# Kernel tuning notes

Measured on AMD Instinct MI355X. Metric: run time of the kernel, lower is better.

## Reference

```python
import jax, jax.numpy as jnp
import numpy as np

B, C, H, W = 8, 128, 64, 64
NWIN, HEADS, QKDIM, KVPW, TOPK = 8, 8, 128, 4, 16
SCALE = QKDIM ** -0.5

def _ln(x, g, b, eps):
    mu = x.mean(-1, keepdims=True)
    var = ((x - mu) ** 2).mean(-1, keepdims=True)
    return (x - mu) * jax.lax.rsqrt(var + eps) * g + b

def _conv(x, w, b, pad, groups=1):
    y = jax.lax.conv_general_dilated(x, w, (1, 1), [(pad, pad), (pad, pad)],
        dimension_numbers=('NCHW', 'OIHW', 'NCHW'), feature_group_count=groups)
    return y + b[None, :, None, None]

def setup_inputs():
    key = jax.random.key(0)
    ks = jax.random.split(key, 8)
    s = 0.05
    return {
        't1': jax.random.normal(ks[0], (B, C, H, W), jnp.float32),
        't2': jax.random.normal(ks[1], (B, C, H, W), jnp.float32),
        'pos_w': jax.random.normal(ks[2], (C, 1, 3, 3), jnp.float32) * s,
        'pos_b': jnp.zeros((C,), jnp.float32),
        'cat_w': jax.random.normal(ks[3], (C, 2 * C, 3, 3), jnp.float32) * s,
        'cat_b': jnp.zeros((C,), jnp.float32),
        'ln_cat_g': jnp.ones((C,), jnp.float32),
        'ln_cat_b': jnp.zeros((C,), jnp.float32),
        'ln1_g': jnp.ones((C,), jnp.float32),
        'ln1_b': jnp.zeros((C,), jnp.float32),
        'qkv_w': jax.random.normal(ks[4], (2 * QKDIM + C, C), jnp.float32) * s,
        'qkv_b': jnp.zeros((2 * QKDIM + C,), jnp.float32),
        'lepe_w': jax.random.normal(ks[5], (C, 1, 5, 5), jnp.float32) * s,
        'lepe_b': jnp.zeros((C,), jnp.float32),
        'wo_w': jax.random.normal(ks[6], (C, C), jnp.float32) * s,
        'wo_b': jnp.zeros((C,), jnp.float32),
    }

def _bra_cross(q_in, kv_in, qkv_w, qkv_b, lepe_w, lepe_b, wo_w, wo_b):
    # Bi-level routing cross attention: queries from q_in, keys/values from kv_in (NHWC).
    p = NWIN; wh, ww = H // p, W // p; p2 = p * p
    q = (q_in @ qkv_w.T + qkv_b)[..., :QKDIM]          # (B,H,W,QKDIM)
    kv = (kv_in @ qkv_w.T + qkv_b)[..., QKDIM:]        # (B,H,W,QKDIM+C)

    def win(x):
        c = x.shape[-1]
        return x.reshape(B, p, wh, p, ww, c).transpose(0, 1, 3, 2, 4, 5).reshape(B, p2, wh, ww, c)

    qw, kvw = win(q), win(kv)
    q_pix = qw.reshape(B, p2, wh * ww, QKDIM)
    # adaptive avg-pool each window's kv to KVPW x KVPW ('ada_avgpool')
    f = wh // KVPW
    kv_pix = kvw.reshape(B, p2, KVPW, f, KVPW, f, QKDIM + C).mean(axis=(3, 5))
    kv_pix = kv_pix.reshape(B, p2, KVPW * KVPW, QKDIM + C)
    q_win = qw.mean(axis=(2, 3))                        # (B,p2,QKDIM)
    k_win = kvw[..., :QKDIM].mean(axis=(2, 3))
    # LePE: depthwise 5x5 conv on full-resolution v
    v_full = kv[..., QKDIM:].transpose(0, 3, 1, 2)
    lepe = _conv(v_full, lepe_w, lepe_b, 2, groups=C).transpose(0, 2, 3, 1)
    # region-level routing (detached: diff_routing=False)
    logits = jnp.einsum('bpc,bqc->bpq',
                        jax.lax.stop_gradient(q_win) * SCALE,
                        jax.lax.stop_gradient(k_win))
    _, r_idx = jax.lax.top_k(logits, TOPK)              # (B,p2,TOPK)
    # gather kv of routed regions: (B,p2,TOPK,KVPW^2,QKDIM+C)
    kv_sel = jax.vmap(lambda kvp, idx: kvp[idx])(kv_pix, r_idx)
    k_sel = kv_sel[..., :QKDIM].reshape(B, p2, TOPK * KVPW * KVPW, HEADS, QKDIM // HEADS)
    v_sel = kv_sel[..., QKDIM:].reshape(B, p2, TOPK * KVPW * KVPW, HEADS, C // HEADS)
    q_h = q_pix.reshape(B, p2, wh * ww, HEADS, QKDIM // HEADS)
    attn = jnp.einsum('bpqmc,bpkmc->bpmqk', q_h * SCALE, k_sel)
    attn = jax.nn.softmax(attn, axis=-1)
    out = jnp.einsum('bpmqk,bpkmc->bpqmc', attn, v_sel).reshape(B, p2, wh, ww, C)
    out = out.reshape(B, p, p, wh, ww, C).transpose(0, 1, 3, 2, 4, 5).reshape(B, H, W, C)
    out = out + lepe
    return out @ wo_w.T + wo_b

def reference(t1, t2, pos_w, pos_b, cat_w, cat_b, ln_cat_g, ln_cat_b,
              ln1_g, ln1_b, qkv_w, qkv_b, lepe_w, lepe_b, wo_w, wo_b):
    # Block.forward: depthwise conv positional embedding
    t1 = t1 + _conv(t1, pos_w, pos_b, 1, groups=C)
    t2 = t2 + _conv(t2, pos_w, pos_b, 1, groups=C)
    t1n = t1.transpose(0, 2, 3, 1)
    t2n = t2.transpose(0, 2, 3, 1)
    # RGBConcatConv: cat on channel-last, 3x3 conv, relu(LayerNorm)
    xc = jnp.concatenate([t1n, t2n], axis=3).transpose(0, 3, 1, 2)
    xc = _conv(xc, cat_w, cat_b, 1).transpose(0, 2, 3, 1)
    x = jax.nn.relu(_ln(xc, ln_cat_g, ln_cat_b, 1e-5))
    attn = _bra_cross(_ln(t1n, ln1_g, ln1_b, 1e-6), _ln(t2n, ln1_g, ln1_b, 1e-6),
                      qkv_w, qkv_b, lepe_w, lepe_b, wo_w, wo_b)
    x = x + attn
    return x.transpose(0, 3, 1, 2)
```

## Files before the change

### kernel.cpp

```cpp
#include <hip/hip_runtime.h>
#include <math.h>

typedef unsigned short ushort_t;
typedef __attribute__((ext_vector_type(4))) float f32x4;
typedef __attribute__((ext_vector_type(16))) float f32x16;
typedef __attribute__((ext_vector_type(8))) short bf16x8;

constexpr int B = 8, C = 128, H = 64, W = 64;
constexpr int HEADS = 8, TOPK = 16;
constexpr int P2 = 64;
constexpr float SCALE = 0.0883883476483184405f;

constexpr size_t NPIX    = (size_t)B * H * W;
constexpr size_t OFF_T1C = 0;
constexpr size_t OFF_T2C = OFF_T1C + NPIX * 128;
constexpr size_t OFF_X   = OFF_T2C + NPIX * 128;
constexpr size_t OFF_QB  = OFF_X   + NPIX * 128;
constexpr size_t OFF_KV  = OFF_QB  + NPIX * 64;
constexpr size_t OFF_KVP = OFF_KV  + NPIX * 256;
constexpr size_t OFF_RW1 = OFF_KVP + 524288;
constexpr size_t OFF_RW2 = OFF_RW1 + 524288;
constexpr size_t OFF_KVPT= OFF_KVP + (size_t)B * P2 * 16 * 256;
constexpr size_t OFF_QW  = OFF_KVPT+ (size_t)B * P2 * 128 * 16 / 2;
constexpr size_t OFF_KW  = OFF_QW  + (size_t)B * P2 * 128;
constexpr size_t OFF_RIDX= OFF_KW  + (size_t)B * P2 * 128;
constexpr size_t OFF_WCB = OFF_RIDX+ (size_t)B * P2 * TOPK;
constexpr size_t OFF_QKVB= OFF_WCB + (size_t)9 * 256 * 128;
constexpr size_t OFF_WOB = OFF_QKVB+ (size_t)384 * 128 / 2;
constexpr size_t OFF_T1B = OFF_WOB + 8192;
constexpr size_t OFF_T2B = OFF_T1B + NPIX * 64;

__device__ inline ushort_t f2bf(float f) {
    unsigned u = __float_as_uint(f);
    unsigned r = u + 0x7FFFu + ((u >> 16) & 1u);
    return (ushort_t)(r >> 16);
}
__device__ inline float bf2f(ushort_t u) {
    return __uint_as_float((unsigned)u << 16);
}

__global__ __launch_bounds__(256) void prep_pos_k(
        const float* __restrict__ t1, const float* __restrict__ t2,
        const float* __restrict__ pos_w, const float* __restrict__ pos_b,
        const float* __restrict__ qkv_w, const float* __restrict__ wo_w,
        const float* __restrict__ cat_w,
        ushort_t* __restrict__ qkvB, ushort_t* __restrict__ woB,
        ushort_t* __restrict__ wcat2,
        float* __restrict__ out1, float* __restrict__ out2,
        ushort_t* __restrict__ ob1, ushort_t* __restrict__ ob2) {
    __shared__ float tile[4][32][33];
    int bid = blockIdx.x;
    int t = threadIdx.x;
    if (bid < 1152) {
        int idx = bid * 256 + t;
        if (idx < 384 * 128) qkvB[idx] = f2bf(qkv_w[idx]);
        if (idx < 128 * 128) woB[idx]  = f2bf(wo_w[idx]);
        if (idx < 36 * 8 * 128 * 8) {
            int i  = idx & 7;
            int n  = (idx >> 3) & 127;
            int r  = idx >> 10;
            int lg = r & 3;
            int kk = (r >> 2) & 1;
            int sdd = r >> 3;
            int dd = sdd % 9, q = sdd / 9;
            int ci = q * 64 + kk * 32 + lg * 8 + i;
            wcat2[idx] = f2bf(cat_w[((size_t)n * 256 + ci) * 9 + dd]);
        }
        return;
    }
    int pb = bid - 1152;
    int xb = pb & 1, cg = (pb >> 1) & 3, z = pb >> 3;
    int which = z >> 7, rem = z & 127;
    int b = rem >> 4, y0 = (rem & 15) * 4;
    const float* in = which ? t2 : t1;
    float* outNHWC = which ? out2 : out1;
    ushort_t* outB = which ? ob2 : ob1;
    int c0 = cg * 32, x0 = xb * 32;
    int tx = t & 31, tg = t >> 5;
    int x = x0 + tx;
    for (int i = 0; i < 4; i++) {
        int cl = tg * 4 + i, c = c0 + cl;
        const float* base = in + (size_t)(b * C + c) * H * W;
        float wv[9];
#pragma unroll
        for (int j = 0; j < 9; j++) wv[j] = pos_w[c * 9 + j];
        float rows[6][3];
#pragma unroll
        for (int yy = 0; yy < 6; yy++) {
            int gy = y0 - 1 + yy;
            bool yok = (gy >= 0 && gy < H);
#pragma unroll
            for (int dx = 0; dx < 3; dx++) {
                int gx = x + dx - 1;
                rows[yy][dx] = (yok && gx >= 0 && gx < W) ? base[gy * W + gx] : 0.f;
            }
        }
        float bb = pos_b[c];
#pragma unroll
        for (int k = 0; k < 4; k++) {
            float acc = rows[k + 1][1] + bb;
#pragma unroll
            for (int dy = 0; dy < 3; dy++)
#pragma unroll
                for (int dx = 0; dx < 3; dx++)
                    acc += rows[k + dy][dx] * wv[dy * 3 + dx];
            tile[k][cl][tx] = acc;
        }
    }
    __syncthreads();
    for (int k = 0; k < 4; k++)
        for (int i = 0; i < 4; i++) {
            int xl = tg * 4 + i;
            float val = tile[k][tx][xl];
            size_t idx = ((size_t)(b * H + y0 + k) * W + x0 + xl) * 128 + c0 + tx;
            outNHWC[idx] = val;
            outB[idx] = f2bf(val);
        }
}

__global__ __launch_bounds__(512) void cat_ln_k(
        const ushort_t* __restrict__ t1b, const ushort_t* __restrict__ t2b,
        const ushort_t* __restrict__ wcat2,
        const float* __restrict__ cat_b,
        const float* __restrict__ gcat, const float* __restrict__ bcat,
        ushort_t* __restrict__ xbuf,
        const float* __restrict__ t1c, const float* __restrict__ t2c,
        const float* __restrict__ g1, const float* __restrict__ b1,
        const ushort_t* __restrict__ qkvB, const float* __restrict__ qkv_b,
        ushort_t* __restrict__ outQ, ushort_t* __restrict__ outKV,
        float* __restrict__ rw1, float* __restrict__ rw2) {
    __shared__ __align__(16) unsigned char smem[64 * 272 * 2];
    int bid = blockIdx.x;
    int t = threadIdx.x;
    int lane = t & 63, wv = t >> 6;
    int l15 = lane & 15, lg = lane >> 4;

    if (bid < 512) {
        unsigned char* ash = smem;
        int which = bid >> 8;
        int blk = bid & 255;
        const float* in = which ? t2c : t1c;
        float* rw = which ? rw2 : rw1;
        size_t p0 = (size_t)blk * 128;
        int bb_ = blk >> 5, y0 = (blk & 31) * 2;
        {
            int row = t >> 2, sub = t & 3;
            const float* src = in + (p0 + row) * 128 + sub * 32;
            float4 v[8];
            float s = 0.f;
#pragma unroll
            for (int j = 0; j < 8; j++) {
                v[j] = *reinterpret_cast<const float4*>(src + j * 4);
                s += v[j].x + v[j].y + v[j].z + v[j].w;
            }
            s += __shfl_xor(s, 1, 64); s += __shfl_xor(s, 2, 64);
            float mean = s * (1.f / 128.f);
            float s2 = 0.f;
#pragma unroll
            for (int j = 0; j < 8; j++) {
                float dx = v[j].x - mean, dy = v[j].y - mean;
                float dz = v[j].z - mean, dw = v[j].w - mean;
                s2 += dx * dx + dy * dy + dz * dz + dw * dw;
            }
            s2 += __shfl_xor(s2, 1, 64); s2 += __shfl_xor(s2, 2, 64);
            float inv = rsqrtf(s2 * (1.f / 128.f) + 1e-6f);
            int wj = (wv & 3) * 2 + (lane >> 5);
            int yy_ = y0 + (wv >> 2);
            bool writer = (lane & 28) == 0;
            float* rwp = rw + (((size_t)(bb_ * 8 + wj) * 64 + yy_) * 128) + sub * 32;
#pragma unroll
            for (int j = 0; j < 8; j++) {
                int c = sub * 32 + j * 4;
                float4 gv = *reinterpret_cast<const float4*>(g1 + c);
                float4 bv = *reinterpret_cast<const float4*>(b1 + c);
                float o0 = (v[j].x - mean) * inv * gv.x + bv.x;
                float o1 = (v[j].y - mean) * inv * gv.y + bv.y;
                float o2 = (v[j].z - mean) * inv * gv.z + bv.z;
                float o3 = (v[j].w - mean) * inv * gv.w + bv.w;
                uint2 pk;
                pk.x = (unsigned)f2bf(o0) | ((unsigned)f2bf(o1) << 16);
                pk.y = (unsigned)f2bf(o2) | ((unsigned)f2bf(o3) << 16);
                *reinterpret_cast<uint2*>(ash + row * 272 + c * 2) = pk;
                float r0 = o0, r1 = o1, r2 = o2, r3 = o3;
#pragma unroll
                for (int m = 4; m <= 16; m <<= 1) {
                    r0 += __shfl_xor(r0, m, 64);
                    r1 += __shfl_xor(r1, m, 64);
                    r2 += __shfl_xor(r2, m, 64);
                    r3 += __shfl_xor(r3, m, 64);
                }
                if (writer)
                    *reinterpret_cast<float4*>(rwp + j * 4) = make_float4(r0, r1, r2, r3);
            }
        }
        __syncthreads();
        int mh = wv >> 2, nw = wv & 3;
        if (which == 0) {
            f32x4 acc[4][2];
#pragma unroll
            for (int mt = 0; mt < 4; mt++)
#pragma unroll
                for (int nn = 0; nn < 2; nn++)
                    acc[mt][nn] = (f32x4){0.f, 0.f, 0.f, 0.f};
#pragma unroll
            for (int ks = 0; ks < 4; ks++) {
                bf16x8 af[4];
#pragma unroll
                for (int mt = 0; mt < 4; mt++)
                    af[mt] = *reinterpret_cast<const bf16x8*>(
                        ash + (mh * 64 + mt * 16 + l15) * 272 + ks * 64 + lg * 16);
#pragma unroll
                for (int nn = 0; nn < 2; nn++) {
                    int n = (nw * 2 + nn) * 16 + l15;
                    bf16x8 bfr = *reinterpret_cast<const bf16x8*>(
                        qkvB + (size_t)n * 128 + ks * 32 + lg * 8);
#pragma unroll
                    for (int mt = 0; mt < 4; mt++)
                        acc[mt][nn] = __builtin_amdgcn_mfma_f32_16x16x32_bf16(
                            af[mt], bfr, acc[mt][nn], 0, 0, 0);
                }
            }
#pragma unroll
            for (int nn = 0; nn < 2; nn++) {
                int cg = (nw * 2 + nn) * 16 + l15;
                float bv = qkv_b[cg];
#pragma unroll
                for (int mt = 0; mt < 4; mt++)
#pragma unroll
                    for (int i = 0; i < 4; i++) {
                        size_t pix = p0 + mh * 64 + mt * 16 + lg * 4 + i;
                        outQ[pix * 128 + cg] = f2bf((acc[mt][nn][i] + bv) * SCALE);
                    }
            }
        } else {
            f32x4 acc[4][4];
#pragma unroll
            for (int mt = 0; mt < 4; mt++)
#pragma unroll
                for (int nn = 0; nn < 4; nn++)
                    acc[mt][nn] = (f32x4){0.f, 0.f, 0.f, 0.f};
#pragma unroll
            for (int ks = 0; ks < 4; ks++) {
                bf16x8 af[4];
#pragma unroll
                for (int mt = 0; mt < 4; mt++)
                    af[mt] = *reinterpret_cast<const bf16x8*>(
                        ash + (mh * 64 + mt * 16 + l15) * 272 + ks * 64 + lg * 16);
#pragma unroll
                for (int nn = 0; nn < 4; nn++) {
                    int n = 128 + (nw * 4 + nn) * 16 + l15;
                    bf16x8 bfr = *reinterpret_cast<const bf16x8*>(
                        qkvB + (size_t)n * 128 + ks * 32 + lg * 8);
#pragma unroll
                    for (int mt = 0; mt < 4; mt++)
                        acc[mt][nn] = __builtin_amdgcn_mfma_f32_16x16x32_bf16(
                            af[mt], bfr, acc[mt][nn], 0, 0, 0);
                }
            }
#pragma unroll
            for (int nn = 0; nn < 4; nn++) {
                int cg = (nw * 4 + nn) * 16 + l15;
                float bv = qkv_b[128 + cg];
#pragma unroll
                for (int mt = 0; mt < 4; mt++)
#pragma unroll
                    for (int i = 0; i < 4; i++) {
                        size_t pix = p0 + mh * 64 + mt * 16 + lg * 4 + i;
                        outKV[pix * 256 + cg] = f2bf(acc[mt][nn][i] + bv);
                    }
            }
        }
        return;
    }

    int cb = bid - 512;
    int mw = wv >> 2, nw = wv & 3;
    int b = cb >> 6, y0 = ((cb >> 3) & 7) * 8, x0 = (cb & 7) * 8;

    f32x4 acc[2][2];
#pragma unroll
    for (int m = 0; m < 2; m++)
#pragma unroll
        for (int cf = 0; cf < 2; cf++)
            acc[m][cf] = (f32x4){0.f, 0.f, 0.f, 0.f};

    int pyA[2], pxA[2];
#pragma unroll
    for (int m = 0; m < 2; m++) {
        int p = mw * 32 + m * 16 + l15;
        pyA[m] = p >> 3; pxA[m] = p & 7;
    }

    for (int q = 0; q < 4; q++) {
        __syncthreads();
        {
            const ushort_t* src = (q < 2 ? t1b : t2b);
            int coff = (q & 1) * 64;
            for (int e = t; e < 800; e += 512) {
                int pix = e >> 3, c8 = e & 7;
                int hy = pix / 10, hx = pix - hy * 10;
                int gy = y0 - 1 + hy, gx = x0 - 1 + hx;
                uint4 v = make_uint4(0u, 0u, 0u, 0u);
                if (gy >= 0 && gy < H && gx >= 0 && gx < W)
                    v = *reinterpret_cast<const uint4*>(
                        src + ((size_t)(b * H + gy) * W + gx) * 128 + coff + c8 * 8);
                *reinterpret_cast<uint4*>(smem + pix * 144 + c8 * 16) = v;
            }
        }
        __syncthreads();
#pragma unroll
        for (int dd = 0; dd < 9; dd++) {
            int dy = dd / 3, dx = dd - dy * 3;
            const ushort_t* wb = wcat2 + ((size_t)((q * 9 + dd) * 8 + lg) * 128) * 8;
            bf16x8 bfr[2][2];
#pragma unroll
            for (int kk = 0; kk < 2; kk++)
#pragma unroll
                for (int cf = 0; cf < 2; cf++)
                    bfr[kk][cf] = *reinterpret_cast<const bf16x8*>(
                        wb + (size_t)kk * 4096 + (nw * 32 + cf * 16 + l15) * 8);
            bf16x8 af[2][2];
#pragma unroll
            for (int m = 0; m < 2; m++)
#pragma unroll
                for (int kk = 0; kk < 2; kk++)
                    af[m][kk] = *reinterpret_cast<const bf16x8*>(
                        smem + ((pyA[m] + dy) * 10 + pxA[m] + dx) * 144 + kk * 64 + lg * 16);
#pragma unroll
            for (int m = 0; m < 2; m++)
#pragma unroll
                for (int cf = 0; cf < 2; cf++)
#pragma unroll
                    for (int kk = 0; kk < 2; kk++)
                        acc[m][cf] = __builtin_amdgcn_mfma_f32_16x16x32_bf16(
                            af[m][kk], bfr[kk][cf], acc[m][cf], 0, 0, 0);
        }
    }

    __syncthreads();
    float* res = (float*)smem;
    float* mstat = (float*)(smem + 64 * 132 * 4);
#pragma unroll
    for (int cf = 0; cf < 2; cf++) {
        int n = nw * 32 + cf * 16 + l15;
        float cbv = cat_b[n];
#pragma unroll
        for (int m = 0; m < 2; m++)
#pragma unroll
            for (int i = 0; i < 4; i++)
                res[(mw * 32 + m * 16 + lg * 4 + i) * 132 + n] = acc[m][cf][i] + cbv;
    }
    __syncthreads();
    {
        int pix = t >> 3, sub = t & 7;
        float s1 = 0.f;
#pragma unroll
        for (int j = 0; j < 16; j++) s1 += res[pix * 132 + sub + j * 8];
        s1 += __shfl_xor(s1, 1, 64);
        s1 += __shfl_xor(s1, 2, 64);
        s1 += __shfl_xor(s1, 4, 64);
        float mean = s1 * (1.f / 128.f);
        float s2 = 0.f;
#pragma unroll
        for (int j = 0; j < 16; j++) {
            float d = res[pix * 132 + sub + j * 8] - mean;
            s2 += d * d;
        }
        s2 += __shfl_xor(s2, 1, 64);
        s2 += __shfl_xor(s2, 2, 64);
        s2 += __shfl_xor(s2, 4, 64);
        float inv = rsqrtf(s2 * (1.f / 128.f) + 1e-5f);
        if (sub == 0) { mstat[pix] = mean; mstat[64 + pix] = inv; }
    }
    __syncthreads();
    {
        int c = t & 127, pg = t >> 7;
        float gg = gcat[c], bb = bcat[c];
        for (int j = 0; j < 16; j++) {
            int p2 = j * 4 + pg;
            float v = (res[p2 * 132 + c] - mstat[p2]) * mstat[64 + p2] * gg + bb;
            int py = p2 >> 3, px = p2 & 7;
            xbuf[((size_t)(b * H + y0 + py) * W + x0 + px) * 128 + c] = f2bf(fmaxf(v, 0.f));
        }
    }
}

__global__ __launch_bounds__(256) void route_pool_k(
        const float* __restrict__ rw1, const float* __restrict__ rw2,
        const float* __restrict__ qkv_w, const float* __restrict__ qkv_b,
        float* __restrict__ qwin, float* __restrict__ kwin,
        const ushort_t* __restrict__ kv,
        ushort_t* __restrict__ kb, ushort_t* __restrict__ kvpT,
        ushort_t* __restrict__ vpl) {
    __shared__ float msh[2][8][128];
    int bid = blockIdx.x;
    int t = threadIdx.x;
    if (bid < 64) {
        int b = bid >> 3, wi = bid & 7;
        for (int i = t; i < 8 * 128; i += 256) {
            int r = i >> 7, c = i & 127;
            size_t off = (((size_t)(b * 8 + r) * 64) + wi * 8) * 128 + c;
            float s1 = 0.f, s2 = 0.f;
#pragma unroll
            for (int rr = 0; rr < 8; rr++) {
                s1 += rw1[off + rr * 128];
                s2 += rw2[off + rr * 128];
            }
            msh[0][r][c] = s1 * (1.f / 64.f);
            msh[1][r][c] = s2 * (1.f / 64.f);
        }
        __syncthreads();
        int c = t;
        int which = c >> 7;
        const float* wrow = qkv_w + (size_t)c * 128;
        float acc[8];
#pragma unroll
        for (int r = 0; r < 8; r++) acc[r] = 0.f;
        for (int k = 0; k < 128; k++) {
            float wv_ = wrow[k];
#pragma unroll
            for (int r = 0; r < 8; r++) acc[r] += msh[which][r][k] * wv_;
        }
        float bv = qkv_b[c];
#pragma unroll
        for (int r = 0; r < 8; r++) {
            size_t o = ((size_t)b * 64 + wi * 8 + r) * 128 + (c & 127);
            (which ? kwin : qwin)[o] = acc[r] + bv;
        }
        return;
    }
    int pb = bid - 64;
    int b = pb >> 6, wdw = pb & 63;
    int wi = wdw >> 3, wj = wdw & 7;
    if (t < 128) {
        float vals[16];
        for (int ry = 0; ry < 4; ry++)
            for (int rx = 0; rx < 4; rx++) {
                float s = 0.f;
                for (int fy = 0; fy < 2; fy++)
                    for (int fx = 0; fx < 2; fx++) {
                        int y = wi * 8 + ry * 2 + fy, x = wj * 8 + rx * 2 + fx;
                        s += bf2f(kv[((size_t)(b * H + y) * W + x) * 256 + t]);
                    }
                vals[ry * 4 + rx] = s * 0.25f;
            }
#pragma unroll
        for (int pos = 0; pos < 16; pos++)
            kb[(((size_t)(b * 64 + wdw)) * 16 + pos) * 128 + t] = f2bf(vals[pos]);
    } else {
        int c = t - 128;
        float ps[4][4];
#pragma unroll
        for (int i = 0; i < 4; i++)
#pragma unroll
            for (int j = 0; j < 4; j++) ps[i][j] = 0.f;
        for (int y = 0; y < 8; y++) {
            union { ushort_t u16[8]; uint4 u4; } raw;
#pragma unroll
            for (int x = 0; x < 8; x++) {
                raw.u16[x] = kv[((size_t)(b * H + wi * 8 + y) * W + wj * 8 + x) * 256 + 128 + c];
                ps[y >> 1][x >> 1] += bf2f(raw.u16[x]);
            }
            *reinterpret_cast<uint4*>(
                vpl + ((size_t)(b * C + c) * H + wi * 8 + y) * W + wj * 8) = raw.u4;
        }
        union { ushort_t u16[16]; uint4 u4[2]; } pk;
#pragma unroll
        for (int ry = 0; ry < 4; ry++)
#pragma unroll
            for (int rx = 0; rx < 4; rx++)
                pk.u16[ry * 4 + rx] = f2bf(ps[ry][rx] * 0.25f);
        size_t base = (((size_t)(b * 64 + wdw)) * 128 + c) * 16;
        *reinterpret_cast<uint4*>(kvpT + base) = pk.u4[0];
        *reinterpret_cast<uint4*>(kvpT + base + 8) = pk.u4[1];
    }
}

__global__ __launch_bounds__(256) void route_lepe_k(
        const float* __restrict__ q_win, const float* __restrict__ k_win,
        int* __restrict__ r_idx,
        const ushort_t* __restrict__ vpl,
        const float* __restrict__ w, const float* __restrict__ bias,
        ushort_t* __restrict__ lep) {
    __shared__ float tile[68][69];
    int bid = blockIdx.x;
    int t = threadIdx.x;
    if (bid < 128) {
        int b = bid >> 4, p = (bid & 15) * 4 + (t >> 6);
        int j = t & 63;
        const float* qp = q_win + (size_t)(b * 64 + p) * 128;
        const float* kp = k_win + (size_t)(b * 64 + j) * 128;
        float lg = 0.f;
        for (int c = 0; c < 128; c++) lg += qp[c] * kp[c];
        lg *= SCALE;
        for (int it = 0; it < TOPK; it++) {
            float v = lg; int idx = j;
#pragma unroll
            for (int m = 32; m > 0; m >>= 1) {
                float ov = __shfl_xor(v, m, 64);
                int   oi = __shfl_xor(idx, m, 64);
                if (ov > v || (ov == v && oi < idx)) { v = ov; idx = oi; }
            }
            if (j == 0) r_idx[(size_t)(b * 64 + p) * TOPK + it] = idx;
            if (j == idx) lg = -__builtin_inff();
        }
        return;
    }
    int lb = bid - 128;
    int c = lb & 127, b = lb >> 7;
    const ushort_t* plane = vpl + (size_t)(b * C + c) * 4096;
    for (int e = t; e < 68 * 68; e += 256) {
        int row = e / 68, col = e - row * 68;
        int gy = row - 2, gx = col - 2;
        tile[row][col] = (gy >= 0 && gy < 64 && gx >= 0 && gx < 64)
                         ? bf2f(plane[gy * 64 + gx]) : 0.f;
    }
    float wv[25];
#pragma unroll
    for (int j = 0; j < 25; j++) wv[j] = w[c * 25 + j];
    float bb = bias[c];
    __syncthreads();
    int y = t >> 2, x0 = (t & 3) * 16;
    float acc[16];
#pragma unroll
    for (int i = 0; i < 16; i++) acc[i] = bb;
#pragma unroll
    for (int dy = 0; dy < 5; dy++) {
        float vals[20];
#pragma unroll
        for (int j = 0; j < 20; j++) vals[j] = tile[y + dy][x0 + j];
#pragma unroll
        for (int dx = 0; dx < 5; dx++)
#pragma unroll
            for (int i = 0; i < 16; i++)
                acc[i] += vals[i + dx] * wv[dy * 5 + dx];
    }
    ushort_t* dst = lep + (size_t)(b * C + c) * 4096 + y * 64 + x0;
    union { ushort_t u16[16]; uint4 u4[2]; } pk;
#pragma unroll
    for (int i = 0; i < 16; i++) pk.u16[i] = f2bf(acc[i]);
    *reinterpret_cast<uint4*>(dst) = pk.u4[0];
    *reinterpret_cast<uint4*>(dst + 8) = pk.u4[1];
}

__global__ __launch_bounds__(256) void attn_mfma_k(
        const ushort_t* __restrict__ qb,
        const ushort_t* __restrict__ kb,
        const ushort_t* __restrict__ kvpT,
        const int* __restrict__ r_idx,
        ushort_t* __restrict__ o) {
    __shared__ int ridx_sh[16];
    __shared__ float denom_sh[4][32];
    __shared__ __align__(16) ushort_t osh[64][32];

    int b = blockIdx.z, p = blockIdx.x, pair = blockIdx.y;
    int wi = p >> 3, wj = p & 7;
    int t = threadIdx.x;
    int lane = t & 63, wv = t >> 6;
    int l31 = lane & 31, hi = lane >> 5;

    if (t < 16) ridx_sh[t] = r_idx[(size_t)(b * 64 + p) * TOPK + t];
    __syncthreads();

    int hh = wv >> 1, qt = wv & 1;
    int h = pair * 2 + hh;

    int q = qt * 32 + l31;
    int qy = wi * 8 + (q >> 3), qx = wj * 8 + (q & 7);
    bf16x8 qf = *reinterpret_cast<const bf16x8*>(
        qb + ((size_t)(b * H + qy) * W + qx) * 128 + h * 16 + hi * 8);

    const ushort_t* kb_b = kb + (size_t)b * 64 * 16 * 128 + h * 16 + hi * 8;
    const ushort_t* vt_b = kvpT + (size_t)b * 64 * 128 * 16 + (h * 16 + (l31 & 15)) * 16 + hi * 8;

    float m_run = -INFINITY, l_run = 0.f;
    f32x16 opv;
#pragma unroll
    for (int r = 0; r < 16; r++) opv[r] = 0.f;
    f32x16 zf;
#pragma unroll
    for (int r = 0; r < 16; r++) zf[r] = 0.f;

    bf16x8 kf = *reinterpret_cast<const bf16x8*>(
        kb_b + ((size_t)ridx_sh[l31 >> 4] * 16 + (l31 & 15)) * 128);
    bf16x8 v0 = *reinterpret_cast<const bf16x8*>(vt_b + (size_t)ridx_sh[0] * 2048);
    bf16x8 v1 = *reinterpret_cast<const bf16x8*>(vt_b + (size_t)ridx_sh[1] * 2048);

    for (int t8 = 0; t8 < 8; t8++) {
        bf16x8 kfn = kf, v0n = v0, v1n = v1;
        if (t8 < 7) {
            kfn = *reinterpret_cast<const bf16x8*>(
                kb_b + ((size_t)ridx_sh[2 * t8 + 2 + (l31 >> 4)] * 16 + (l31 & 15)) * 128);
            v0n = *reinterpret_cast<const bf16x8*>(vt_b + (size_t)ridx_sh[2 * t8 + 2] * 2048);
            v1n = *reinterpret_cast<const bf16x8*>(vt_b + (size_t)ridx_sh[2 * t8 + 3] * 2048);
        }
        f32x16 S = __builtin_amdgcn_mfma_f32_32x32x16_bf16(kf, qf, zf, 0, 0, 0);
        float tm = S[0];
#pragma unroll
        for (int r = 1; r < 16; r++) tm = fmaxf(tm, S[r]);
        tm = fmaxf(tm, __shfl_xor(tm, 32, 64));
        float m_new = fmaxf(m_run, tm);
        float corr = __expf(m_run - m_new);
        float p_[16], psum = 0.f;
#pragma unroll
        for (int r = 0; r < 16; r++) { p_[r] = __expf(S[r] - m_new); psum += p_[r]; }
        psum += __shfl_xor(psum, 32, 64);
        l_run = l_run * corr + psum;
        m_run = m_new;
#pragma unroll
        for (int r = 0; r < 16; r++) opv[r] *= corr;
        unsigned w_[8], pw_[8];
#pragma unroll
        for (int j = 0; j < 8; j++)
            w_[j] = (__float_as_uint(p_[2 * j]) >> 16) |
                    (__float_as_uint(p_[2 * j + 1]) & 0xFFFF0000u);
#pragma unroll
        for (int j = 0; j < 8; j++) pw_[j] = __shfl_xor(w_[j], 32, 64);
        union { unsigned u[4]; bf16x8 v; } fa0, fa1;
        fa0.u[0] = hi ? pw_[2] : w_[0];
        fa0.u[1] = hi ? pw_[3] : w_[1];
        fa0.u[2] = hi ? w_[2]  : pw_[0];
        fa0.u[3] = hi ? w_[3]  : pw_[1];
        fa1.u[0] = hi ? pw_[6] : w_[4];
        fa1.u[1] = hi ? pw_[7] : w_[5];
        fa1.u[2] = hi ? w_[6]  : pw_[4];
        fa1.u[3] = hi ? w_[7]  : pw_[5];
        opv = __builtin_amdgcn_mfma_f32_32x32x16_bf16(fa0.v, v0, opv, 0, 0, 0);
        opv = __builtin_amdgcn_mfma_f32_32x32x16_bf16(fa1.v, v1, opv, 0, 0, 0);
        kf = kfn; v0 = v0n; v1 = v1n;
    }
    denom_sh[wv][l31] = l_run;
    if (l31 < 16) {
#pragma unroll
        for (int r = 0; r < 16; r++) {
            int qr = (r & 3) + 8 * (r >> 2) + 4 * hi;
            float invd = 1.f / denom_sh[wv][qr];
            osh[qt * 32 + qr][hh * 16 + l31] = f2bf(opv[r] * invd);
        }
    }
    __syncthreads();
    {
        int p_ = t >> 2, seg = t & 3;
        int y = wi * 8 + (p_ >> 3), x = wj * 8 + (p_ & 7);
        *reinterpret_cast<uint4*>(
            o + ((size_t)(b * H + y) * W + x) * 128 + pair * 32 + seg * 8) =
            *reinterpret_cast<const uint4*>(&osh[p_][seg * 8]);
    }
}

__global__ __launch_bounds__(256) void epilogue_mfma_k(
        const ushort_t* __restrict__ o,
        const ushort_t* __restrict__ lep,
        const ushort_t* __restrict__ xbuf,
        const ushort_t* __restrict__ woB,
        const float* __restrict__ wo_b,
        float* __restrict__ out) {
    __shared__ __align__(16) unsigned char smem[128 * 68 * 4];
    ushort_t* ash = (ushort_t*)smem;
    float* res = (float*)smem;
    int t = threadIdx.x, lane = t & 63, wv = t >> 6;
    int bid = blockIdx.x;
    int b = bid >> 6, y = bid & 63;
    size_t p0 = (size_t)bid * 64;

#pragma unroll
    for (int k = 0; k < 4; k++) {
        int e = k * 256 + t;
        int c = e >> 3, xg = e & 7;
        union { uint4 u4; ushort_t u16[8]; } v;
        v.u4 = *reinterpret_cast<const uint4*>(
            lep + (((size_t)(b * C + c) * 64 + y) * 64) + xg * 8);
#pragma unroll
        for (int j = 0; j < 8; j++) ash[(xg * 8 + j) * 136 + c] = v.u16[j];
    }
    __syncthreads();
    {
        int x = t >> 2, sub = t & 3;
        const ushort_t* op = o + (p0 + x) * 128 + sub * 32;
        ushort_t* ap = ash + x * 136 + sub * 32;
#pragma unroll
        for (int jj = 0; jj < 4; jj++) {
            union { uint4 u4; ushort_t u16[8]; } ov, lv;
            ov.u4 = *reinterpret_cast<const uint4*>(op + jj * 8);
            lv.u4 = *reinterpret_cast<const uint4*>(ap + jj * 8);
#pragma unroll
            for (int j = 0; j < 8; j++)
                lv.u16[j] = f2bf(bf2f(ov.u16[j]) + bf2f(lv.u16[j]));
            *reinterpret_cast<uint4*>(ap + jj * 8) = lv.u4;
        }
    }
    __syncthreads();
    int l15 = lane & 15, lg = lane >> 4;
    f32x4 acc[4][2];
#pragma unroll
    for (int mt = 0; mt < 4; mt++)
#pragma unroll
        for (int nn = 0; nn < 2; nn++)
            acc[mt][nn] = (f32x4){0.f, 0.f, 0.f, 0.f};
#pragma unroll
    for (int ks = 0; ks < 4; ks++) {
        bf16x8 af[4];
#pragma unroll
        for (int mt = 0; mt < 4; mt++)
            af[mt] = *reinterpret_cast<const bf16x8*>(
                ash + (mt * 16 + l15) * 136 + ks * 32 + lg * 8);
#pragma unroll
        for (int nn = 0; nn < 2; nn++) {
            int n = (wv * 2 + nn) * 16 + l15;
            bf16x8 bfr = *reinterpret_cast<const bf16x8*>(
                woB + (size_t)n * 128 + ks * 32 + lg * 8);
#pragma unroll
            for (int mt = 0; mt < 4; mt++)
                acc[mt][nn] = __builtin_amdgcn_mfma_f32_16x16x32_bf16(
                    af[mt], bfr, acc[mt][nn], 0, 0, 0);
        }
    }
    __syncthreads();
#pragma unroll
    for (int nn = 0; nn < 2; nn++) {
        int n = (wv * 2 + nn) * 16 + l15;
        float wb = wo_b[n];
#pragma unroll
        for (int mt = 0; mt < 4; mt++)
#pragma unroll
            for (int i = 0; i < 4; i++) {
                int r = mt * 16 + lg * 4 + i;
                float xb = bf2f(xbuf[(p0 + r) * 128 + n]);
                res[n * 68 + r] = acc[mt][nn][i] + wb + xb;
            }
    }
    __syncthreads();
    {
        int c = t >> 1, x0 = (t & 1) * 32;
        float* dst = out + ((size_t)(b * C + c) * 64 + y) * 64 + x0;
#pragma unroll
        for (int gblk = 0; gblk < 8; gblk++)
            *reinterpret_cast<float4*>(dst + gblk * 4) =
                *reinterpret_cast<const float4*>(&res[c * 68 + x0 + gblk * 4]);
    }
}

extern "C" void kernel_launch(void* const* d_in, const int* in_sizes, int n_in,
                              void* d_out, int out_size, void* d_ws, size_t ws_size,
                              hipStream_t stream) {
    const float* t1      = (const float*)d_in[0];
    const float* t2      = (const float*)d_in[1];
    const float* pos_w   = (const float*)d_in[2];
    const float* pos_b   = (const float*)d_in[3];
    const float* cat_w   = (const float*)d_in[4];
    const float* cat_b   = (const float*)d_in[5];
    const float* ln_cat_g= (const float*)d_in[6];
    const float* ln_cat_b= (const float*)d_in[7];
    const float* ln1_g   = (const float*)d_in[8];
    const float* ln1_b   = (const float*)d_in[9];
    const float* qkv_w   = (const float*)d_in[10];
    const float* qkv_b   = (const float*)d_in[11];
    const float* lepe_w  = (const float*)d_in[12];
    const float* lepe_b  = (const float*)d_in[13];
    const float* wo_w    = (const float*)d_in[14];
    const float* wo_b    = (const float*)d_in[15];

    float* ws    = (float*)d_ws;
    float* t1c   = ws + OFF_T1C;
    float* t2c   = ws + OFF_T2C;
    ushort_t* xbuf = (ushort_t*)(ws + OFF_X);
    ushort_t* qbuf = (ushort_t*)(ws + OFF_QB);
    ushort_t* kvbuf= (ushort_t*)(ws + OFF_KV);
    ushort_t* kb   = (ushort_t*)(ws + OFF_KVP);
    float* rw1   = ws + OFF_RW1;
    float* rw2   = ws + OFF_RW2;
    ushort_t* kvpT = (ushort_t*)(ws + OFF_KVPT);
    float* qwin  = ws + OFF_QW;
    float* kwin  = ws + OFF_KW;
    int*   ridx  = (int*)(ws + OFF_RIDX);
    ushort_t* wcat2 = (ushort_t*)(ws + OFF_WCB);
    ushort_t* qkvB  = (ushort_t*)(ws + OFF_QKVB);
    ushort_t* woB   = (ushort_t*)(ws + OFF_WOB);
    ushort_t* t1b   = (ushort_t*)(ws + OFF_T1B);
    ushort_t* t2b   = (ushort_t*)(ws + OFF_T2B);
    ushort_t* obuf  = (ushort_t*)(ws + OFF_T1C);
    ushort_t* vpl   = (ushort_t*)(ws + OFF_T2C);
    ushort_t* lep   = (ushort_t*)(ws + OFF_KV);
    float* out   = (float*)d_out;

    prep_pos_k<<<3200, 256, 0, stream>>>(
        t1, t2, pos_w, pos_b, qkv_w, wo_w, cat_w,
        qkvB, woB, wcat2, t1c, t2c, t1b, t2b);
    cat_ln_k<<<1024, 512, 0, stream>>>(
        t1b, t2b, wcat2, cat_b, ln_cat_g, ln_cat_b, xbuf,
        t1c, t2c, ln1_g, ln1_b, qkvB, qkv_b, qbuf, kvbuf, rw1, rw2);
    route_pool_k<<<576, 256, 0, stream>>>(
        rw1, rw2, qkv_w, qkv_b, qwin, kwin, kvbuf, kb, kvpT, vpl);
    route_lepe_k<<<1152, 256, 0, stream>>>(
        qwin, kwin, ridx, vpl, lepe_w, lepe_b, lep);
    attn_mfma_k<<<dim3(64, 4, B), 256, 0, stream>>>(qbuf, kb, kvpT, ridx, obuf);
    epilogue_mfma_k<<<512, 256, 0, stream>>>(obuf, lep, xbuf, woB, wo_b, out);
}
```

Before: 157.8 us.

## Restructure cat_ln kernel: 256-thread blocks, register-prefetched conv, fused LN stats

The fused kernel now uses 256-thread blocks with a 1536-block grid, and puts the 3x3 concat-conv blocks first and the LN+QKV blocks after them. The conv no longer stages a halo tile in shared memory. Each wave loads its A and B fragments straight from global memory into registers, double-buffered one tap ahead, so the per-q __syncthreads barriers go away. The LayerNorm after the conv computes sum and sum-of-squares from the accumulators with shuffles, replacing the full fp32 result tile in LDS, and rows are written out with 16-byte vector stores. The trade-offs are redundant global/L2 reads of overlapping halo pixels, higher register pressure, and a one-pass variance formula that is slightly less numerically robust.

```diff
diff --git a/kernel.cpp b/kernel.cpp
--- a/kernel.cpp
+++ b/kernel.cpp
@@ -118,7 +118,7 @@
         }
 }
 
-__global__ __launch_bounds__(512) void cat_ln_k(
+__global__ __launch_bounds__(256) void cat_ln_k(
         const ushort_t* __restrict__ t1b, const ushort_t* __restrict__ t2b,
         const ushort_t* __restrict__ wcat2,
         const float* __restrict__ cat_b,
@@ -129,258 +129,276 @@
         const ushort_t* __restrict__ qkvB, const float* __restrict__ qkv_b,
         ushort_t* __restrict__ outQ, ushort_t* __restrict__ outKV,
         float* __restrict__ rw1, float* __restrict__ rw2) {
-    __shared__ __align__(16) unsigned char smem[64 * 272 * 2];
+    __shared__ __align__(16) unsigned char smem[19456];
     int bid = blockIdx.x;
     int t = threadIdx.x;
     int lane = t & 63, wv = t >> 6;
     int l15 = lane & 15, lg = lane >> 4;
 
     if (bid < 512) {
-        unsigned char* ash = smem;
-        int which = bid >> 8;
-        int blk = bid & 255;
-        const float* in = which ? t2c : t1c;
-        float* rw = which ? rw2 : rw1;
-        size_t p0 = (size_t)blk * 128;
-        int bb_ = blk >> 5, y0 = (blk & 31) * 2;
-        {
-            int row = t >> 2, sub = t & 3;
-            const float* src = in + (p0 + row) * 128 + sub * 32;
-            float4 v[8];
-            float s = 0.f;
-#pragma unroll
-            for (int j = 0; j < 8; j++) {
-                v[j] = *reinterpret_cast<const float4*>(src + j * 4);
-                s += v[j].x + v[j].y + v[j].z + v[j].w;
-            }
-            s += __shfl_xor(s, 1, 64); s += __shfl_xor(s, 2, 64);
-            float mean = s * (1.f / 128.f);
-            float s2 = 0.f;
-#pragma unroll
-            for (int j = 0; j < 8; j++) {
-                float dx = v[j].x - mean, dy = v[j].y - mean;
-                float dz = v[j].z - mean, dw = v[j].w - mean;
-                s2 += dx * dx + dy * dy + dz * dz + dw * dw;
-            }
-            s2 += __shfl_xor(s2, 1, 64); s2 += __shfl_xor(s2, 2, 64);
-            float inv = rsqrtf(s2 * (1.f / 128.f) + 1e-6f);
-            int wj = (wv & 3) * 2 + (lane >> 5);
-            int yy_ = y0 + (wv >> 2);
-            bool writer = (lane & 28) == 0;
-            float* rwp = rw + (((size_t)(bb_ * 8 + wj) * 64 + yy_) * 128) + sub * 32;
-#pragma unroll
-            for (int j = 0; j < 8; j++) {
-                int c = sub * 32 + j * 4;
-                float4 gv = *reinterpret_cast<const float4*>(g1 + c);
-                float4 bv = *reinterpret_cast<const float4*>(b1 + c);
-                float o0 = (v[j].x - mean) * inv * gv.x + bv.x;
-                float o1 = (v[j].y - mean) * inv * gv.y + bv.y;
-                float o2 = (v[j].z - mean) * inv * gv.z + bv.z;
-                float o3 = (v[j].w - mean) * inv * gv.w + bv.w;
-                uint2 pk;
-                pk.x = (unsigned)f2bf(o0) | ((unsigned)f2bf(o1) << 16);
-                pk.y = (unsigned)f2bf(o2) | ((unsigned)f2bf(o3) << 16);
-                *reinterpret_cast<uint2*>(ash + row * 272 + c * 2) = pk;
-                float r0 = o0, r1 = o1, r2 = o2, r3 = o3;
-#pragma unroll
-                for (int m = 4; m <= 16; m <<= 1) {
-                    r0 += __shfl_xor(r0, m, 64);
-                    r1 += __shfl_xor(r1, m, 64);
-                    r2 += __shfl_xor(r2, m, 64);
-                    r3 += __shfl_xor(r3, m, 64);
+        int cb = bid;
+        int mw = wv >> 1, nw = wv & 1;
+        int b = cb >> 6, y0 = ((cb >> 3) & 7) * 8, x0 = (cb & 7) * 8;
+        int bH = b * 64;
+        int pyA[2], pxA[2];
+#pragma unroll
+        for (int mt = 0; mt < 2; mt++) {
+            int p = mw * 32 + mt * 16 + l15;
+            pyA[mt] = y0 + (p >> 3); pxA[mt] = x0 + (p & 7);
+        }
+        bf16x8 zv = {0, 0, 0, 0, 0, 0, 0, 0};
+
+        f32x4 acc[2][4];
+#pragma unroll
+        for (int mt = 0; mt < 2; mt++)
+#pragma unroll
+            for (int cf = 0; cf < 4; cf++)
+                acc[mt][cf] = (f32x4){0.f, 0.f, 0.f, 0.f};
+
+        auto loadA = [&](int q, int dd, bf16x8 (&Af)[2][2]) {
+            const ushort_t* src = (q < 2) ? t1b : t2b;
+            int coff = (q & 1) * 64;
+            int dy = dd / 3 - 1, dx = dd - (dd / 3) * 3 - 1;
+#pragma unroll
+            for (int mt = 0; mt < 2; mt++) {
+                int gy = pyA[mt] + dy, gx = pxA[mt] + dx;
+                bool ok = ((unsigned)gy < 64u) && ((unsigned)gx < 64u);
+                int gyc = gy < 0 ? 0 : (gy > 63 ? 63 : gy);
+                int gxc = gx < 0 ? 0 : (gx > 63 ? 63 : gx);
+                const ushort_t* p = src + ((size_t)(bH + gyc) * 64 + gxc) * 128
+                                        + coff + lg * 8;
+#pragma unroll
+                for (int kk = 0; kk < 2; kk++) {
+                    bf16x8 v = *reinterpret_cast<const bf16x8*>(p + kk * 32);
+                    Af[mt][kk] = ok ? v : zv;
                 }
-                if (writer)
-                    *reinterpret_cast<float4*>(rwp + j * 4) = make_float4(r0, r1, r2, r3);
-            }
-        }
+            }
+        };
+        auto loadB = [&](int q, int dd, bf16x8 (&Bf)[2][4]) {
+            const ushort_t* wb = wcat2 + ((size_t)((q * 9 + dd) * 8 + lg) * 128) * 8;
+#pragma unroll
+            for (int kk = 0; kk < 2; kk++)
+#pragma unroll
+                for (int cf = 0; cf < 4; cf++)
+                    Bf[kk][cf] = *reinterpret_cast<const bf16x8*>(
+                        wb + (size_t)kk * 4096 + (nw * 64 + cf * 16 + l15) * 8);
+        };
+
+        bf16x8 Ac[2][2], Bc[2][4], An[2][2], Bn[2][4];
+        loadA(0, 0, Ac); loadB(0, 0, Bc);
+        for (int q = 0; q < 4; q++) {
+#pragma unroll
+            for (int dd = 0; dd < 9; dd++) {
+                if (dd < 8)      { loadA(q, dd + 1, An); loadB(q, dd + 1, Bn); }
+                else if (q < 3)  { loadA(q + 1, 0, An);  loadB(q + 1, 0, Bn);  }
+#pragma unroll
+                for (int mt = 0; mt < 2; mt++)
+#pragma unroll
+                    for (int cf = 0; cf < 4; cf++)
+#pragma unroll
+                        for (int kk = 0; kk < 2; kk++)
+                            acc[mt][cf] = __builtin_amdgcn_mfma_f32_16x16x32_bf16(
+                                Ac[mt][kk], Bc[kk][cf], acc[mt][cf], 0, 0, 0);
+#pragma unroll
+                for (int mt = 0; mt < 2; mt++)
+#pragma unroll
+                    for (int kk = 0; kk < 2; kk++) Ac[mt][kk] = An[mt][kk];
+#pragma unroll
+                for (int kk = 0; kk < 2; kk++)
+#pragma unroll
+                    for (int cf = 0; cf < 4; cf++) Bc[kk][cf] = Bn[kk][cf];
+            }
+        }
+
+        float* psum  = (float*)smem;
+        float* psum2 = (float*)(smem + 1024);
+        ushort_t* xsh = (ushort_t*)(smem + 2048);
+        float gv[4], bvv[4];
+#pragma unroll
+        for (int cf = 0; cf < 4; cf++) {
+            int n = nw * 64 + cf * 16 + l15;
+            float cbv = cat_b[n];
+            gv[cf] = gcat[n]; bvv[cf] = bcat[n];
+#pragma unroll
+            for (int mt = 0; mt < 2; mt++)
+#pragma unroll
+                for (int i = 0; i < 4; i++) acc[mt][cf][i] += cbv;
+        }
+#pragma unroll
+        for (int mt = 0; mt < 2; mt++)
+#pragma unroll
+            for (int i = 0; i < 4; i++) {
+                float s = 0.f, s2 = 0.f;
+#pragma unroll
+                for (int cf = 0; cf < 4; cf++) {
+                    float v = acc[mt][cf][i];
+                    s += v; s2 += v * v;
+                }
+                s  += __shfl_xor(s, 1, 64);  s2 += __shfl_xor(s2, 1, 64);
+                s  += __shfl_xor(s, 2, 64);  s2 += __shfl_xor(s2, 2, 64);
+                s  += __shfl_xor(s, 4, 64);  s2 += __shfl_xor(s2, 4, 64);
+                s  += __shfl_xor(s, 8, 64);  s2 += __shfl_xor(s2, 8, 64);
+                int p = mw * 32 + mt * 16 + lg * 4 + i;
+                if (l15 == 0) { psum[wv * 64 + p] = s; psum2[wv * 64 + p] = s2; }
+            }
         __syncthreads();
-        int mh = wv >> 2, nw = wv & 3;
-        if (which == 0) {
-            f32x4 acc[4][2];
+#pragma unroll
+        for (int mt = 0; mt < 2; mt++)
+#pragma unroll
+            for (int i = 0; i < 4; i++) {
+                int p = mw * 32 + mt * 16 + lg * 4 + i;
+                float tot  = psum[(mw * 2) * 64 + p]  + psum[(mw * 2 + 1) * 64 + p];
+                float tot2 = psum2[(mw * 2) * 64 + p] + psum2[(mw * 2 + 1) * 64 + p];
+                float mean = tot * (1.f / 128.f);
+                float inv = rsqrtf(tot2 * (1.f / 128.f) - mean * mean + 1e-5f);
+#pragma unroll
+                for (int cf = 0; cf < 4; cf++) {
+                    float v = (acc[mt][cf][i] - mean) * inv * gv[cf] + bvv[cf];
+                    xsh[p * 136 + nw * 64 + cf * 16 + l15] = f2bf(fmaxf(v, 0.f));
+                }
+            }
+        __syncthreads();
+        for (int e = t; e < 1024; e += 256) {
+            int pix = e >> 4, c16 = e & 15;
+            int gy = y0 + (pix >> 3), gx = x0 + (pix & 7);
+            *reinterpret_cast<uint4*>(
+                xbuf + ((size_t)(bH + gy) * 64 + gx) * 128 + c16 * 8) =
+                *reinterpret_cast<const uint4*>(xsh + pix * 136 + c16 * 8);
+        }
+        return;
+    }
+
+    unsigned char* ash = smem;
+    int lb = bid - 512;
+    int which = lb >> 9;
+    int blk = lb & 511;
+    const float* in = which ? t2c : t1c;
+    float* rw = which ? rw2 : rw1;
+    size_t p0 = (size_t)blk * 64;
+    int bb_ = blk >> 6, yy_ = blk & 63;
+    {
+        int row = t >> 2, sub = t & 3;
+        const float* src = in + (p0 + row) * 128 + sub * 32;
+        float4 v[8];
+        float s = 0.f;
+#pragma unroll
+        for (int j = 0; j < 8; j++) {
+            v[j] = *reinterpret_cast<const float4*>(src + j * 4);
+            s += v[j].x + v[j].y + v[j].z + v[j].w;
+        }
+        s += __shfl_xor(s, 1, 64); s += __shfl_xor(s, 2, 64);
+        float mean = s * (1.f / 128.f);
+        float s2 = 0.f;
+#pragma unroll
+        for (int j = 0; j < 8; j++) {
+            float dx = v[j].x - mean, dy = v[j].y - mean;
+            float dz = v[j].z - mean, dw = v[j].w - mean;
+            s2 += dx * dx + dy * dy + dz * dz + dw * dw;
+        }
+        s2 += __shfl_xor(s2, 1, 64); s2 += __shfl_xor(s2, 2, 64);
+        float inv = rsqrtf(s2 * (1.f / 128.f) + 1e-6f);
+        int wj = wv * 2 + (lane >> 5);
+        bool writer = (lane & 28) == 0;
+        float* rwp = rw + (((size_t)(bb_ * 8 + wj) * 64 + yy_) * 128) + sub * 32;
+#pragma unroll
+        for (int j = 0; j < 8; j++) {
+            int c = sub * 32 + j * 4;
+            float4 gv = *reinterpret_cast<const float4*>(g1 + c);
+            float4 bv = *reinterpret_cast<const float4*>(b1 + c);
+            float o0 = (v[j].x - mean) * inv * gv.x + bv.x;
+            float o1 = (v[j].y - mean) * inv * gv.y + bv.y;
+            float o2 = (v[j].z - mean) * inv * gv.z + bv.z;
+            float o3 = (v[j].w - mean) * inv * gv.w + bv.w;
+            uint2 pk;
+            pk.x = (unsigned)f2bf(o0) | ((unsigned)f2bf(o1) << 16);
+            pk.y = (unsigned)f2bf(o2) | ((unsigned)f2bf(o3) << 16);
+            *reinterpret_cast<uint2*>(ash + row * 272 + c * 2) = pk;
+            float r0 = o0, r1 = o1, r2 = o2, r3 = o3;
+#pragma unroll
+            for (int m = 4; m <= 16; m <<= 1) {
+                r0 += __shfl_xor(r0, m, 64);
+                r1 += __shfl_xor(r1, m, 64);
+                r2 += __shfl_xor(r2, m, 64);
+                r3 += __shfl_xor(r3, m, 64);
+            }
+            if (writer)
+                *reinterpret_cast<float4*>(rwp + j * 4) = make_float4(r0, r1, r2, r3);
+        }
+    }
+    __syncthreads();
+    if (which == 0) {
+        f32x4 acc[4][2];
+#pragma unroll
+        for (int mt = 0; mt < 4; mt++)
+#pragma unroll
+            for (int nn = 0; nn < 2; nn++)
+                acc[mt][nn] = (f32x4){0.f, 0.f, 0.f, 0.f};
+#pragma unroll
+        for (int ks = 0; ks < 4; ks++) {
+            bf16x8 af[4];
 #pragma unroll
             for (int mt = 0; mt < 4; mt++)
-#pragma unroll
-                for (int nn = 0; nn < 2; nn++)
-                    acc[mt][nn] = (f32x4){0.f, 0.f, 0.f, 0.f};
-#pragma unroll
-            for (int ks = 0; ks < 4; ks++) {
-                bf16x8 af[4];
+                af[mt] = *reinterpret_cast<const bf16x8*>(
+                    ash + (mt * 16 + l15) * 272 + ks * 64 + lg * 16);
+#pragma unroll
+            for (int nn = 0; nn < 2; nn++) {
+                int n = (wv * 2 + nn) * 16 + l15;
+                bf16x8 bfr = *reinterpret_cast<const bf16x8*>(
+                    qkvB + (size_t)n * 128 + ks * 32 + lg * 8);
 #pragma unroll
                 for (int mt = 0; mt < 4; mt++)
-                    af[mt] = *reinterpret_cast<const bf16x8*>(
-                        ash + (mh * 64 + mt * 16 + l15) * 272 + ks * 64 + lg * 16);
-#pragma unroll
-                for (int nn = 0; nn < 2; nn++) {
-                    int n = (nw * 2 + nn) * 16 + l15;
-                    bf16x8 bfr = *reinterpret_cast<const bf16x8*>(
-                        qkvB + (size_t)n * 128 + ks * 32 + lg * 8);
-#pragma unroll
-                    for (int mt = 0; mt < 4; mt++)
-                        acc[mt][nn] = __builtin_amdgcn_mfma_f32_16x16x32_bf16(
-                            af[mt], bfr, acc[mt][nn], 0, 0, 0);
+                    acc[mt][nn] = __builtin_amdgcn_mfma_f32_16x16x32_bf16(
+                        af[mt], bfr, acc[mt][nn], 0, 0, 0);
+            }
+        }
+#pragma unroll
+        for (int nn = 0; nn < 2; nn++) {
+            int cg = (wv * 2 + nn) * 16 + l15;
+            float bv = qkv_b[cg];
+#pragma unroll
+            for (int mt = 0; mt < 4; mt++)
+#pragma unroll
+                for (int i = 0; i < 4; i++) {
+                    size_t pix = p0 + mt * 16 + lg * 4 + i;
+                    outQ[pix * 128 + cg] = f2bf((acc[mt][nn][i] + bv) * SCALE);
                 }
-            }
-#pragma unroll
-            for (int nn = 0; nn < 2; nn++) {
-                int cg = (nw * 2 + nn) * 16 + l15;
-                float bv = qkv_b[cg];
+        }
+    } else {
+        f32x4 acc[4][4];
+#pragma unroll
+        for (int mt = 0; mt < 4; mt++)
+#pragma unroll
+            for (int nn = 0; nn < 4; nn++)
+                acc[mt][nn] = (f32x4){0.f, 0.f, 0.f, 0.f};
+#pragma unroll
+        for (int ks = 0; ks < 4; ks++) {
+            bf16x8 af[4];
+#pragma unroll
+            for (int mt = 0; mt < 4; mt++)
+                af[mt] = *reinterpret_cast<const bf16x8*>(
+                    ash + (mt * 16 + l15) * 272 + ks * 64 + lg * 16);
+#pragma unroll
+            for (int nn = 0; nn < 4; nn++) {
+                int n = 128 + (wv * 4 + nn) * 16 + l15;
+                bf16x8 bfr = *reinterpret_cast<const bf16x8*>(
+                    qkvB + (size_t)n * 128 + ks * 32 + lg * 8);
 #pragma unroll
                 for (int mt = 0; mt < 4; mt++)
-#pragma unroll
-                    for (int i = 0; i < 4; i++) {
-                        size_t pix = p0 + mh * 64 + mt * 16 + lg * 4 + i;
-                        outQ[pix * 128 + cg] = f2bf((acc[mt][nn][i] + bv) * SCALE);
-                    }
-            }
-        } else {
-            f32x4 acc[4][4];
+                    acc[mt][nn] = __builtin_amdgcn_mfma_f32_16x16x32_bf16(
+                        af[mt], bfr, acc[mt][nn], 0, 0, 0);
+            }
+        }
+#pragma unroll
+        for (int nn = 0; nn < 4; nn++) {
+            int cg = (wv * 4 + nn) * 16 + l15;
+            float bv = qkv_b[128 + cg];
 #pragma unroll
             for (int mt = 0; mt < 4; mt++)
 #pragma unroll
-                for (int nn = 0; nn < 4; nn++)
-                    acc[mt][nn] = (f32x4){0.f, 0.f, 0.f, 0.f};
-#pragma unroll
-            for (int ks = 0; ks < 4; ks++) {
-                bf16x8 af[4];
-#pragma unroll
-                for (int mt = 0; mt < 4; mt++)
-                    af[mt] = *reinterpret_cast<const bf16x8*>(
-                        ash + (mh * 64 + mt * 16 + l15) * 272 + ks * 64 + lg * 16);
-#pragma unroll
-                for (int nn = 0; nn < 4; nn++) {
-                    int n = 128 + (nw * 4 + nn) * 16 + l15;
-                    bf16x8 bfr = *reinterpret_cast<const bf16x8*>(
-                        qkvB + (size_t)n * 128 + ks * 32 + lg * 8);
-#pragma unroll
-                    for (int mt = 0; mt < 4; mt++)
-                        acc[mt][nn] = __builtin_amdgcn_mfma_f32_16x16x32_bf16(
-                            af[mt], bfr, acc[mt][nn], 0, 0, 0);
+                for (int i = 0; i < 4; i++) {
+                    size_t pix = p0 + mt * 16 + lg * 4 + i;
+                    outKV[pix * 256 + cg] = f2bf(acc[mt][nn][i] + bv);
                 }
-            }
-#pragma unroll
-            for (int nn = 0; nn < 4; nn++) {
-                int cg = (nw * 4 + nn) * 16 + l15;
-                float bv = qkv_b[128 + cg];
-#pragma unroll
-                for (int mt = 0; mt < 4; mt++)
-#pragma unroll
-                    for (int i = 0; i < 4; i++) {
-                        size_t pix = p0 + mh * 64 + mt * 16 + lg * 4 + i;
-                        outKV[pix * 256 + cg] = f2bf(acc[mt][nn][i] + bv);
-                    }
-            }
-        }
-        return;
-    }
-
-    int cb = bid - 512;
-    int mw = wv >> 2, nw = wv & 3;
-    int b = cb >> 6, y0 = ((cb >> 3) & 7) * 8, x0 = (cb & 7) * 8;
-
-    f32x4 acc[2][2];
-#pragma unroll
-    for (int m = 0; m < 2; m++)
-#pragma unroll
-        for (int cf = 0; cf < 2; cf++)
-            acc[m][cf] = (f32x4){0.f, 0.f, 0.f, 0.f};
-
-    int pyA[2], pxA[2];
-#pragma unroll
-    for (int m = 0; m < 2; m++) {
-        int p = mw * 32 + m * 16 + l15;
-        pyA[m] = p >> 3; pxA[m] = p & 7;
-    }
-
-    for (int q = 0; q < 4; q++) {
-        __syncthreads();
-        {
-            const ushort_t* src = (q < 2 ? t1b : t2b);
-            int coff = (q & 1) * 64;
-            for (int e = t; e < 800; e += 512) {
-                int pix = e >> 3, c8 = e & 7;
-                int hy = pix / 10, hx = pix - hy * 10;
-                int gy = y0 - 1 + hy, gx = x0 - 1 + hx;
-                uint4 v = make_uint4(0u, 0u, 0u, 0u);
-                if (gy >= 0 && gy < H && gx >= 0 && gx < W)
-                    v = *reinterpret_cast<const uint4*>(
-                        src + ((size_t)(b * H + gy) * W + gx) * 128 + coff + c8 * 8);
-                *reinterpret_cast<uint4*>(smem + pix * 144 + c8 * 16) = v;
-            }
-        }
-        __syncthreads();
-#pragma unroll
-        for (int dd = 0; dd < 9; dd++) {
-            int dy = dd / 3, dx = dd - dy * 3;
-            const ushort_t* wb = wcat2 + ((size_t)((q * 9 + dd) * 8 + lg) * 128) * 8;
-            bf16x8 bfr[2][2];
-#pragma unroll
-            for (int kk = 0; kk < 2; kk++)
-#pragma unroll
-                for (int cf = 0; cf < 2; cf++)
-                    bfr[kk][cf] = *reinterpret_cast<const bf16x8*>(
-                        wb + (size_t)kk * 4096 + (nw * 32 + cf * 16 + l15) * 8);
-            bf16x8 af[2][2];
-#pragma unroll
-            for (int m = 0; m < 2; m++)
-#pragma unroll
-                for (int kk = 0; kk < 2; kk++)
-                    af[m][kk] = *reinterpret_cast<const bf16x8*>(
-                        smem + ((pyA[m] + dy) * 10 + pxA[m] + dx) * 144 + kk * 64 + lg * 16);
-#pragma unroll
-            for (int m = 0; m < 2; m++)
-#pragma unroll
-                for (int cf = 0; cf < 2; cf++)
-#pragma unroll
-                    for (int kk = 0; kk < 2; kk++)
-                        acc[m][cf] = __builtin_amdgcn_mfma_f32_16x16x32_bf16(
-                            af[m][kk], bfr[kk][cf], acc[m][cf], 0, 0, 0);
-        }
-    }
-
-    __syncthreads();
-    float* res = (float*)smem;
-    float* mstat = (float*)(smem + 64 * 132 * 4);
-#pragma unroll
-    for (int cf = 0; cf < 2; cf++) {
-        int n = nw * 32 + cf * 16 + l15;
-        float cbv = cat_b[n];
-#pragma unroll
-        for (int m = 0; m < 2; m++)
-#pragma unroll
-            for (int i = 0; i < 4; i++)
-                res[(mw * 32 + m * 16 + lg * 4 + i) * 132 + n] = acc[m][cf][i] + cbv;
-    }
-    __syncthreads();
-    {
-        int pix = t >> 3, sub = t & 7;
-        float s1 = 0.f;
-#pragma unroll
-        for (int j = 0; j < 16; j++) s1 += res[pix * 132 + sub + j * 8];
-        s1 += __shfl_xor(s1, 1, 64);
-        s1 += __shfl_xor(s1, 2, 64);
-        s1 += __shfl_xor(s1, 4, 64);
-        float mean = s1 * (1.f / 128.f);
-        float s2 = 0.f;
-#pragma unroll
-        for (int j = 0; j < 16; j++) {
-            float d = res[pix * 132 + sub + j * 8] - mean;
-            s2 += d * d;
-        }
-        s2 += __shfl_xor(s2, 1, 64);
-        s2 += __shfl_xor(s2, 2, 64);
-        s2 += __shfl_xor(s2, 4, 64);
-        float inv = rsqrtf(s2 * (1.f / 128.f) + 1e-5f);
-        if (sub == 0) { mstat[pix] = mean; mstat[64 + pix] = inv; }
-    }
-    __syncthreads();
-    {
-        int c = t & 127, pg = t >> 7;
-        float gg = gcat[c], bb = bcat[c];
-        for (int j = 0; j < 16; j++) {
-            int p2 = j * 4 + pg;
-            float v = (res[p2 * 132 + c] - mstat[p2]) * mstat[64 + p2] * gg + bb;
-            int py = p2 >> 3, px = p2 & 7;
-            xbuf[((size_t)(b * H + y0 + py) * W + x0 + px) * 128 + c] = f2bf(fmaxf(v, 0.f));
         }
     }
 }
@@ -786,7 +804,7 @@
     prep_pos_k<<<3200, 256, 0, stream>>>(
         t1, t2, pos_w, pos_b, qkv_w, wo_w, cat_w,
         qkvB, woB, wcat2, t1c, t2c, t1b, t2b);
-    cat_ln_k<<<1024, 512, 0, stream>>>(
+    cat_ln_k<<<1536, 256, 0, stream>>>(
         t1b, t2b, wcat2, cat_b, ln_cat_g, ln_cat_b, xbuf,
         t1c, t2c, ln1_g, ln1_b, qkvB, qkv_b, qbuf, kvbuf, rw1, rw2);
     route_pool_k<<<576, 256, 0, stream>>>(
```

Measured after the change: 168.0 us. +6.5%, slower.
